# Kernel optimization log

Hardware: AMD Instinct MI355X
Metric: run time of the kernel (lower is better)

Reference implementation:

```python
import jax, jax.numpy as jnp
import numpy as np

# Hardware-emulation constants (from init_kwargs, NeuroSim-style QLinear)
WL_IN = 8        # input activation bit width (bit-serial)
WL_W = 8         # weight bit width
CELL_BIT = 2     # bits per memory cell -> 4 weight slices
SUB = 128        # crossbar sub-array size (rows summed in analog)
ADC_BITS = 5     # ADC precision per partial sum
ONOFF = 10.0     # cell on/off conductance ratio
VARI = 0.05      # multiplicative device variation sigma


def _adc_quant(x, bits, axes):
    # LinearQuantizeOut: uniform quantization between tensor min/max
    mn = jnp.min(x, axis=axes, keepdims=True)
    mx = jnp.max(x, axis=axes, keepdims=True)
    step = (mx - mn) * (2.0 ** (-bits))
    step = jnp.where(step <= 0, 1.0, step)
    idx = jnp.clip(jnp.floor((x - mn) / step), 0.0, 2.0 ** bits - 1.0)
    return idx * step + mn


def _qlinear_hw(x, w, noise):
    """Analog PIM crossbar emulation of y = x @ w.T with bit-serial inputs,
    bit-sliced cells, on/off-ratio offset + dummy column, device variation,
    per-subarray ADC quantization."""
    B, N = x.shape
    F = w.shape[0]
    I, W, K = WL_IN, WL_W, WL_W // CELL_BIT
    cr = 2.0 ** CELL_BIT
    lower, upper = 1.0 / ONOFF, 1.0
    S = (N + SUB - 1) // SUB
    Np = S * SUB
    # quantize input to I bits in [0,1]; weight to W-bit integer in [0, 2^W-1]
    xq = jnp.round(jnp.clip(x, 0.0, 1.0) * (2.0 ** I - 1.0))            # [B, N]
    Xi = jnp.clip(jnp.round((w + 1.0) * 0.5 * (2.0 ** W - 1.0)), 0.0, 2.0 ** W - 1.0)  # [F, N]
    xq = jnp.pad(xq, ((0, 0), (0, Np - N)))
    Xi = jnp.pad(Xi, ((0, 0), (0, Np - N)))
    zpow = 2.0 ** jnp.arange(I, dtype=x.dtype)
    kpow = cr ** jnp.arange(K, dtype=x.dtype)
    bits = jnp.mod(jnp.floor(xq[..., None] / zpow), 2.0)                # [B, Np, I]
    slc = jnp.mod(jnp.floor(Xi[..., None] / kpow), cr)                  # [F, Np, K]
    g = slc * (upper - lower) + (cr - 1.0) * lower                      # cell conductances
    g = g * (1.0 + VARI * noise)                                        # device variation
    bits = bits.reshape(B, S, SUB, I)
    g = g.reshape(F, S, SUB, K)
    # analog partial sums per (input bit i, subarray s, weight slice k)
    P = jnp.einsum('bsai,fsak->iskbf', bits, g)                         # [I,S,K,B,F]
    # dummy column (all cells at lowest conductance), identical across F
    D = jnp.transpose(bits.sum(axis=2), (2, 1, 0)) * ((cr - 1.0) * lower)  # [I,S,B]
    Pq = _adc_quant(P, ADC_BITS, axes=(3, 4))
    Dq = _adc_quant(D, ADC_BITS, axes=(2,))
    scal = (2.0 ** jnp.arange(I, dtype=x.dtype))[:, None] * (cr ** jnp.arange(K, dtype=x.dtype))[None, :]
    acc = jnp.einsum('iskbf,ik->bf', Pq - Dq[:, :, None, :, None], scal) / (upper - lower)
    # undo integer mappings: w = 2*Xi/(2^W-1) - 1, x = xq/(2^I-1)
    out = 2.0 * acc / ((2.0 ** I - 1.0) * (2.0 ** W - 1.0)) \
          - xq.sum(axis=1, keepdims=True) / (2.0 ** I - 1.0)
    return out


def _qlinear(x, w, noise):
    # straight-through quantized weight (WAGE-style STE) + hardware forward
    Xi = jnp.clip(jnp.round((w + 1.0) * 0.5 * (2.0 ** WL_W - 1.0)), 0.0, 2.0 ** WL_W - 1.0)
    wq = 2.0 * Xi / (2.0 ** WL_W - 1.0) - 1.0
    wq_ste = w + jax.lax.stop_gradient(wq - w)
    out_ideal = x @ wq_ste.T
    out_hw = _qlinear_hw(x, w, noise)
    return out_ideal + jax.lax.stop_gradient(out_hw - out_ideal)


def setup_inputs() -> dict:
    key = jax.random.key(0)
    k1, k2, k3, k4, k5 = jax.random.split(key, 5)
    x = jax.random.uniform(k1, (1024, 784), dtype=jnp.float32)
    w1 = jax.random.normal(k2, (512, 784), dtype=jnp.float32) * 0.05
    w3 = jax.random.normal(k3, (10, 512), dtype=jnp.float32) * 0.08
    noise1 = jax.random.normal(k4, (512, 896, 4), dtype=jnp.float32)  # 784 padded to 7*128
    noise3 = jax.random.normal(k5, (10, 512, 4), dtype=jnp.float32)   # 512 = 4*128 exact
    return {"x": x, "w1": w1, "w3": w3, "noise1": noise1, "noise3": noise3}


def reference(x, w1, w3, noise1, noise3):
    h = jnp.tanh(_qlinear(x, w1, noise1))   # QLinear(784,512) + Tanh
    return _qlinear(h, w3, noise3)          # QLinear(512,10)
```

## Files before the change

kernel.cpp:

```cpp
#include <hip/hip_runtime.h>

#define FLTMAX 3.402823466e+38f


__global__ void prep1_kernel(const float* __restrict__ x, float* __restrict__ sx1,
                             unsigned* __restrict__ xqbT, unsigned* __restrict__ stats1)
{
    __shared__ float xr[896];
    __shared__ float red[128];
    int b = blockIdx.x;
    if (b == 0) {
        for (int t = threadIdx.x; t < 224; t += 128) {
            stats1[t * 2] = 0x7F7FFFFFu; stats1[t * 2 + 1] = 0u;
        }
    }
    float psum = 0.f;
    for (int n = threadIdx.x; n < 896; n += 128) {
        float v = 0.f;
        if (n < 784) {
            float xv = x[b * 784 + n];
            xv = fminf(fmaxf(xv, 0.f), 1.f);
            v = rintf(__fmul_rn(xv, 255.f));
        }
        xr[n] = v;
        psum += v;
    }
    red[threadIdx.x] = psum;
    __syncthreads();
    for (int w = 64; w >= 1; w >>= 1) {
        if (threadIdx.x < w) red[threadIdx.x] += red[threadIdx.x + w];
        __syncthreads();
    }
    if (threadIdx.x == 0) sx1[b] = red[0];
    if (threadIdx.x < 28) {
        int w = threadIdx.x;
        unsigned words[8] = {0, 0, 0, 0, 0, 0, 0, 0};
#pragma unroll 8
        for (int n = 0; n < 32; ++n) {
            int v = (int)xr[w * 32 + n];
#pragma unroll
            for (int i = 0; i < 8; ++i) words[i] |= ((unsigned)((v >> i) & 1)) << n;
        }
#pragma unroll
        for (int i = 0; i < 8; ++i) xqbT[(i * 28 + w) * 1024 + b] = words[i];
    }
}

__global__ void prepg1t_kernel(const float* __restrict__ w1, const float* __restrict__ noise1,
                               float* __restrict__ g1t)
{
    __shared__ float t[4][32][33];
    const int n0 = blockIdx.x * 32, f0 = blockIdx.y * 32;
    const int tid = threadIdx.x;
    {
        int n = tid & 31, fi = tid >> 5;
#pragma unroll
        for (int p = 0; p < 4; ++p) {
            int f = p * 8 + fi;
            int gn = n0 + n, gf = f0 + f;
            float gv[4] = {0.f, 0.f, 0.f, 0.f};
            if (gn < 784) {
                float w = w1[gf * 784 + gn];
                float Xi = fminf(fmaxf(rintf(__fmul_rn(__fmul_rn(__fadd_rn(w, 1.f), 0.5f), 255.f)),
                                       0.f), 255.f);
                int xi = (int)Xi;
                float4 nz = *(const float4*)&noise1[(gf * 896 + gn) * 4];
                float nzv[4] = {nz.x, nz.y, nz.z, nz.w};
#pragma unroll
                for (int k = 0; k < 4; ++k) {
                    int slc = (xi >> (2 * k)) & 3;
                    float base = __fadd_rn(__fmul_rn((float)slc, 0.9f), 0.3f);
                    float nf = __fadd_rn(1.f, __fmul_rn(0.05f, nzv[k]));
                    gv[k] = __fmul_rn(base, nf);
                }
            }
#pragma unroll
            for (int k = 0; k < 4; ++k) t[k][n][f] = gv[k];
        }
    }
    __syncthreads();
    {
        int f = tid & 31, nn = tid >> 5;
#pragma unroll
        for (int p = 0; p < 4; ++p) {
            int n = p * 8 + nn;
#pragma unroll
            for (int k = 0; k < 4; ++k)
                g1t[(n0 + n) * 2048 + k * 512 + f0 + f] = t[k][n][f];
        }
    }
}

__global__ void prepg2_kernel(const float* __restrict__ w3, const float* __restrict__ noise3,
                              float* __restrict__ g2t)
{
    int gid = blockIdx.x * 256 + threadIdx.x;
    if (gid >= 10 * 512) return;
    int f = gid / 512, n = gid % 512;
    float w = w3[f * 512 + n];
    float Xi = fminf(fmaxf(rintf(__fmul_rn(__fmul_rn(__fadd_rn(w, 1.f), 0.5f), 255.f)),
                           0.f), 255.f);
    int xi = (int)Xi;
#pragma unroll
    for (int k = 0; k < 4; ++k) {
        int slc = (xi >> (2 * k)) & 3;
        float base = __fadd_rn(__fmul_rn((float)slc, 0.9f), 0.3f);
        float nf = __fadd_rn(1.f, __fmul_rn(0.05f, noise3[(f * 512 + n) * 4 + k]));
        g2t[n * 40 + k * 10 + f] = __fmul_rn(base, nf);
    }
}

__global__ void dqpopT_kernel(const unsigned* __restrict__ xqbT, float* __restrict__ Dq)
{
    __shared__ float red[512];
    const int i = blockIdx.x / 7, s = blockIdx.x % 7;
    const int tid = threadIdx.x;
    float D[4];
    float mn = FLTMAX, mx = -FLTMAX;
#pragma unroll
    for (int u = 0; u < 4; ++u) {
        int b = tid + u * 256;
        int c = 0;
#pragma unroll
        for (int w = 0; w < 4; ++w)
            c += __popc(xqbT[(i * 28 + s * 4 + w) * 1024 + b]);
        D[u] = __fmul_rn((float)c, 0.3f);
        mn = fminf(mn, D[u]);
        mx = fmaxf(mx, D[u]);
    }
    red[tid] = mn; red[256 + tid] = mx;
    __syncthreads();
    for (int w = 128; w >= 1; w >>= 1) {
        if (tid < w) {
            red[tid] = fminf(red[tid], red[tid + w]);
            red[256 + tid] = fmaxf(red[256 + tid], red[256 + tid + w]);
        }
        __syncthreads();
    }
    mn = red[0]; mx = red[256];
    float step = __fmul_rn(__fsub_rn(mx, mn), 0.03125f);
    if (step <= 0.f) step = 1.f;
#pragma unroll
    for (int u = 0; u < 4; ++u) {
        int b = tid + u * 256;
        float idx = fminf(fmaxf(floorf(__fdiv_rn(__fsub_rn(D[u], mn), step)), 0.f), 31.f);
        Dq[(i * 7 + s) * 1024 + b] = __fadd_rn(__fmul_rn(idx, step), mn);
    }
}

__global__ void dqpop_kernel(const unsigned* __restrict__ xqb, float* __restrict__ Dq,
                             int S, int wpr)
{
    __shared__ float red[512];
    const int i = blockIdx.x / S, s = blockIdx.x % S;
    const int tid = threadIdx.x;
    float D[4];
    float mn = FLTMAX, mx = -FLTMAX;
#pragma unroll
    for (int u = 0; u < 4; ++u) {
        int b = tid + u * 256;
        uint4 w = *(const uint4*)&xqb[(i * 1024 + b) * wpr + s * 4];
        int c = __popc(w.x) + __popc(w.y) + __popc(w.z) + __popc(w.w);
        D[u] = __fmul_rn((float)c, 0.3f);
        mn = fminf(mn, D[u]);
        mx = fmaxf(mx, D[u]);
    }
    red[tid] = mn; red[256 + tid] = mx;
    __syncthreads();
    for (int w = 128; w >= 1; w >>= 1) {
        if (tid < w) {
            red[tid] = fminf(red[tid], red[tid + w]);
            red[256 + tid] = fmaxf(red[256 + tid], red[256 + tid + w]);
        }
        __syncthreads();
    }
    mn = red[0]; mx = red[256];
    float step = __fmul_rn(__fsub_rn(mx, mn), 0.03125f);
    if (step <= 0.f) step = 1.f;
#pragma unroll
    for (int u = 0; u < 4; ++u) {
        int b = tid + u * 256;
        float idx = fminf(fmaxf(floorf(__fdiv_rn(__fsub_rn(D[u], mn), step)), 0.f), 31.f);
        Dq[(i * S + s) * 1024 + b] = __fadd_rn(__fmul_rn(idx, step), mn);
    }
}

__global__ void dterm_kernel(const float* __restrict__ Dq, float* __restrict__ dterm, int S)
{
    int b = blockIdx.x * 256 + threadIdx.x;
    if (b >= 1024) return;
    float sum = 0.f;
    for (int i = 0; i < 8; ++i) {
        float sc = (float)(85 << i);
        for (int s = 0; s < S; ++s) sum = fmaf(Dq[(i * S + s) * 1024 + b], sc, sum);
    }
    dterm[b] = sum;
}

#define BK 32
__global__ __launch_bounds__(256, 4) void mm1_kernel(
    const unsigned* __restrict__ xqbT, const float* __restrict__ g1t,
    float* __restrict__ P, unsigned* __restrict__ stats, int s0)
{
    __shared__ __align__(16) float Bs[BK][132];
    __shared__ unsigned Abits[128];
    __shared__ float red[512];
    const int tid = threadIdx.x;
    const int sl = blockIdx.x >> 6;
    const int r = blockIdx.x & 63;
    const int i = r >> 3;
    const int b0 = (r & 7) * 128;
    const int s = s0 + sl;
    const int colBase = blockIdx.y * 128;
    const int tx = tid & 15, ty = tid >> 4;

    const int aB = tid >> 5;
    const int eB = (tid & 31) << 2;

    float4 pB[4];
    unsigned pAw = 0;
#pragma unroll
    for (int u = 0; u < 4; ++u)
        pB[u] = *(const float4*)&g1t[(s * 128 + u * 8 + aB) * 2048 + colBase + eB];
    if (tid < 128) pAw = xqbT[(i * 28 + s * 4) * 1024 + b0 + tid];

    float acc[8][8] = {};

    for (int ac = 0; ac < 4; ++ac) {
        __syncthreads();
#pragma unroll
        for (int u = 0; u < 4; ++u)
            *(float4*)&Bs[u * 8 + aB][eB] = pB[u];
        if (tid < 128) Abits[tid] = pAw;
        __syncthreads();

        if (ac < 3) {
            const int n0 = s * 128 + (ac + 1) * BK;
#pragma unroll
            for (int u = 0; u < 4; ++u)
                pB[u] = *(const float4*)&g1t[(n0 + u * 8 + aB) * 2048 + colBase + eB];
            if (tid < 128) pAw = xqbT[(i * 28 + s * 4 + ac + 1) * 1024 + b0 + tid];
        }

        unsigned wrd[8];
#pragma unroll
        for (int u = 0; u < 4; ++u) {
            wrd[u]     = Abits[(ty << 2) + u];
            wrd[4 + u] = Abits[64 + (ty << 2) + u];
        }

#pragma unroll 4
        for (int a = 0; a < BK; ++a) {
            float br[8];
            *(float4*)&br[0] = *(const float4*)&Bs[a][(tx << 2)];
            *(float4*)&br[4] = *(const float4*)&Bs[a][64 + (tx << 2)];
#pragma unroll
            for (int u = 0; u < 8; ++u) {
                float ab = (float)((wrd[u] >> a) & 1u);
#pragma unroll
                for (int v = 0; v < 8; ++v)
                    acc[u][v] = fmaf(ab, br[v], acc[u][v]);
            }
        }
    }

#pragma unroll
    for (int uh = 0; uh < 2; ++uh)
#pragma unroll
        for (int u = 0; u < 4; ++u) {
            int row = (sl * 8 + i) * 1024 + b0 + uh * 64 + (ty << 2) + u;
#pragma unroll
            for (int vh = 0; vh < 2; ++vh) {
                float4 v = make_float4(acc[uh * 4 + u][vh * 4 + 0], acc[uh * 4 + u][vh * 4 + 1],
                                       acc[uh * 4 + u][vh * 4 + 2], acc[uh * 4 + u][vh * 4 + 3]);
                *(float4*)&P[(size_t)row * 2048 + colBase + vh * 64 + (tx << 2)] = v;
            }
        }

    float mn = acc[0][0], mx = acc[0][0];
#pragma unroll
    for (int u = 0; u < 8; ++u)
#pragma unroll
        for (int v = 0; v < 8; ++v) { mn = fminf(mn, acc[u][v]); mx = fmaxf(mx, acc[u][v]); }
    red[tid] = mn; red[256 + tid] = mx;
    __syncthreads();
    for (int w = 128; w >= 1; w >>= 1) {
        if (tid < w) {
            red[tid] = fminf(red[tid], red[tid + w]);
            red[256 + tid] = fmaxf(red[256 + tid], red[256 + tid + w]);
        }
        __syncthreads();
    }
    if (tid == 0) {
        int k = colBase >> 9;
        int slot = ((s * 8 + i) * 4 + k) * 2;
        atomicMin(&stats[slot], __float_as_uint(red[0]));
        atomicMax(&stats[slot + 1], __float_as_uint(red[256]));
    }
}

__global__ void quant1_kernel(const float* __restrict__ P, const unsigned* __restrict__ stats,
                              float* __restrict__ acc1, int s0, int G, int first)
{
    int gid = blockIdx.x * 256 + threadIdx.x;
    int b = gid >> 7, f4 = gid & 127;
    float4 accR;
    if (first) accR = make_float4(0.f, 0.f, 0.f, 0.f);
    else       accR = *(const float4*)&acc1[(b << 9) + (f4 << 2)];
    for (int sl = 0; sl < G; ++sl) {
        int s = s0 + sl;
        float4 sum = make_float4(0.f, 0.f, 0.f, 0.f);
        for (int i = 0; i < 8; ++i) {
#pragma unroll
            for (int k = 0; k < 4; ++k) {
                int slot = ((s * 8 + i) * 4 + k) * 2;
                float mn = __uint_as_float(stats[slot]);
                float mx = __uint_as_float(stats[slot + 1]);
                float step = __fmul_rn(__fsub_rn(mx, mn), 0.03125f);
                if (step <= 0.f) step = 1.f;
                float4 val = *(const float4*)&P[(size_t)((sl * 8 + i) * 1024 + b) * 2048
                                                + (k << 9) + (f4 << 2)];
                float sc = (float)(1 << (i + 2 * k));
                float ix, pq;
                ix = fminf(fmaxf(floorf(__fdiv_rn(__fsub_rn(val.x, mn), step)), 0.f), 31.f);
                pq = __fadd_rn(__fmul_rn(ix, step), mn); sum.x = fmaf(pq, sc, sum.x);
                ix = fminf(fmaxf(floorf(__fdiv_rn(__fsub_rn(val.y, mn), step)), 0.f), 31.f);
                pq = __fadd_rn(__fmul_rn(ix, step), mn); sum.y = fmaf(pq, sc, sum.y);
                ix = fminf(fmaxf(floorf(__fdiv_rn(__fsub_rn(val.z, mn), step)), 0.f), 31.f);
                pq = __fadd_rn(__fmul_rn(ix, step), mn); sum.z = fmaf(pq, sc, sum.z);
                ix = fminf(fmaxf(floorf(__fdiv_rn(__fsub_rn(val.w, mn), step)), 0.f), 31.f);
                pq = __fadd_rn(__fmul_rn(ix, step), mn); sum.w = fmaf(pq, sc, sum.w);
            }
        }
        accR.x = __fadd_rn(accR.x, sum.x);
        accR.y = __fadd_rn(accR.y, sum.y);
        accR.z = __fadd_rn(accR.z, sum.z);
        accR.w = __fadd_rn(accR.w, sum.w);
    }
    *(float4*)&acc1[(b << 9) + (f4 << 2)] = accR;
}

__global__ void finish1_kernel(const float* __restrict__ acc1, const float* __restrict__ dterm1,
                               const float* __restrict__ sx1, float* __restrict__ xq2,
                               unsigned* __restrict__ xqb2, float* __restrict__ sx2)
{
    __shared__ float red[512];
    int b = blockIdx.x;
    int f = threadIdx.x;
    int gid = b * 512 + f;
    float total = __fsub_rn(acc1[gid], dterm1[b]);
    float acc = __fdiv_rn(total, 0.9f);
    float o = __fsub_rn(__fdiv_rn(__fmul_rn(2.f, acc), 65025.f), __fdiv_rn(sx1[b], 255.f));
    float h = tanhf(o);
    h = fminf(fmaxf(h, 0.f), 1.f);
    float code = rintf(__fmul_rn(h, 255.f));
    xq2[gid] = code;
    int ci = (int)code;
    int lane = f & 63;
#pragma unroll
    for (int i = 0; i < 8; ++i) {
        unsigned long long m = __ballot((ci >> i) & 1);
        if ((lane & 31) == 0) {
            unsigned wv = (lane & 32) ? (unsigned)(m >> 32) : (unsigned)m;
            xqb2[(i * 1024 + b) * 16 + (f >> 5)] = wv;
        }
    }
    red[f] = code;
    __syncthreads();
    for (int w = 256; w >= 1; w >>= 1) {
        if (f < w) red[f] += red[f + w];
        __syncthreads();
    }
    if (f == 0) sx2[b] = red[0];
}

__global__ void mm2_kernel(const float* __restrict__ xq2, const float* __restrict__ g2t,
                           float* __restrict__ P2)
{
    int gid = blockIdx.x * 256 + threadIdx.x;
    if (gid >= 40960) return;
    int f = gid % 10;
    int b = (gid / 10) & 1023;
    int s = gid / 10240;
    float acc[8][4] = {};
    for (int a = 0; a < 128; ++a) {
        int n = s * 128 + a;
        int xi = (int)xq2[b * 512 + n];
        float g0 = g2t[n * 40 + f];
        float gA = g2t[n * 40 + 10 + f];
        float gB = g2t[n * 40 + 20 + f];
        float gC = g2t[n * 40 + 30 + f];
#pragma unroll
        for (int i = 0; i < 8; ++i) {
            float bi = (float)((xi >> i) & 1);
            acc[i][0] = fmaf(bi, g0, acc[i][0]);
            acc[i][1] = fmaf(bi, gA, acc[i][1]);
            acc[i][2] = fmaf(bi, gB, acc[i][2]);
            acc[i][3] = fmaf(bi, gC, acc[i][3]);
        }
    }
#pragma unroll
    for (int i = 0; i < 8; ++i)
#pragma unroll
        for (int k = 0; k < 4; ++k)
            P2[(size_t)((s * 8 + i) * 4 + k) * 10240 + b * 10 + f] = acc[i][k];
}

__global__ void stat2_kernel(const float* __restrict__ P2, float2* __restrict__ stats2)
{
    __shared__ float red[512];
    int p = blockIdx.x;
    int tid = threadIdx.x;
    float mn = FLTMAX, mx = -FLTMAX;
    for (int t = tid; t < 10240; t += 256) {
        float v = P2[(size_t)p * 10240 + t];
        mn = fminf(mn, v); mx = fmaxf(mx, v);
    }
    red[tid] = mn; red[256 + tid] = mx;
    __syncthreads();
    for (int w = 128; w >= 1; w >>= 1) {
        if (tid < w) {
            red[tid] = fminf(red[tid], red[tid + w]);
            red[256 + tid] = fmaxf(red[256 + tid], red[256 + tid + w]);
        }
        __syncthreads();
    }
    if (tid == 0) {
        float step = __fmul_rn(__fsub_rn(red[256], red[0]), 0.03125f);
        if (step <= 0.f) step = 1.f;
        stats2[p] = make_float2(red[0], step);
    }
}

__global__ void out2_kernel(const float* __restrict__ P2, const float2* __restrict__ stats2,
                            const float* __restrict__ dterm2, const float* __restrict__ sx2,
                            float* __restrict__ out)
{
    int gid = blockIdx.x * 256 + threadIdx.x;
    if (gid >= 10240) return;
    int b = gid / 10;
    float sum = 0.f;
    for (int s = 0; s < 4; ++s)
        for (int i = 0; i < 8; ++i)
#pragma unroll
            for (int k = 0; k < 4; ++k) {
                int p = (s * 8 + i) * 4 + k;
                float2 st = stats2[p];
                float val = P2[(size_t)p * 10240 + gid];
                float idx = fminf(fmaxf(floorf(__fdiv_rn(__fsub_rn(val, st.x), st.y)), 0.f), 31.f);
                float pq = __fadd_rn(__fmul_rn(idx, st.y), st.x);
                sum = fmaf(pq, (float)(1 << (i + 2 * k)), sum);
            }
    float total = __fsub_rn(sum, dterm2[b]);
    float acc = __fdiv_rn(total, 0.9f);
    out[gid] = __fsub_rn(__fdiv_rn(__fmul_rn(2.f, acc), 65025.f), __fdiv_rn(sx2[b], 255.f));
}

extern "C" void kernel_launch(void* const* d_in, const int* in_sizes, int n_in,
                              void* d_out, int out_size, void* d_ws, size_t ws_size,
                              hipStream_t stream)
{
    const float* x      = (const float*)d_in[0];
    const float* w1     = (const float*)d_in[1];
    const float* w3     = (const float*)d_in[2];
    const float* noise1 = (const float*)d_in[3];
    const float* noise3 = (const float*)d_in[4];
    float* out = (float*)d_out;
    float* ws  = (float*)d_ws;

    float*    g1t    = ws + 0;
    float*    acc1   = ws + 1835008;
    float*    xq2    = ws + 2359296;
    float*    P2     = ws + 2883584;
    float*    g2t    = ws + 4194304;
    float*    Dq1    = ws + 4214784;
    float*    Dq2    = ws + 4272128;
    float*    sx1    = ws + 4304896;
    float*    sx2    = ws + 4305920;
    float*    dterm1 = ws + 4306944;
    float*    dterm2 = ws + 4307968;
    float2*   stats2 = (float2*)(ws + 4308992);
    unsigned* stats1 = (unsigned*)(ws + 4309248);
    unsigned* xqbT   = (unsigned*)(ws + 4309760);
    unsigned* xqb2   = (unsigned*)(ws + 4539136);
    float*    Ps     = ws + 4670208;

    const size_t fixedf = 4670208;
    const size_t planef = 16777216;
    int G = ((fixedf + 2 * planef) * sizeof(float) <= ws_size) ? 2 : 1;

    prep1_kernel<<<1024, 128, 0, stream>>>(x, sx1, xqbT, stats1);
    prepg1t_kernel<<<dim3(28, 16), 256, 0, stream>>>(w1, noise1, g1t);
    dqpopT_kernel<<<56, 256, 0, stream>>>(xqbT, Dq1);
    dterm_kernel<<<4, 256, 0, stream>>>(Dq1, dterm1, 7);

    for (int s0 = 0; s0 < 7; s0 += G) {
        int Gc = (7 - s0 < G) ? (7 - s0) : G;
        mm1_kernel<<<dim3(Gc * 64, 16), 256, 0, stream>>>(xqbT, g1t, Ps, stats1, s0);
        quant1_kernel<<<512, 256, 0, stream>>>(Ps, stats1, acc1, s0, Gc, s0 == 0);
    }

    finish1_kernel<<<1024, 512, 0, stream>>>(acc1, dterm1, sx1, xq2, xqb2, sx2);
    prepg2_kernel<<<20, 256, 0, stream>>>(w3, noise3, g2t);
    dqpop_kernel<<<32, 256, 0, stream>>>(xqb2, Dq2, 4, 16);
    dterm_kernel<<<4, 256, 0, stream>>>(Dq2, dterm2, 4);
    mm2_kernel<<<160, 256, 0, stream>>>(xq2, g2t, P2);
    stat2_kernel<<<128, 256, 0, stream>>>(P2, stats2);
    out2_kernel<<<40, 256, 0, stream>>>(P2, stats2, dterm2, sx2, out);
}
```

Measured before the change: 670.4 us.

## Fuse dterm and last quant pass into finish kernels, grow subarray group size

Removes the two dterm kernels by computing the dummy-column term inside finish1 (one thread per row) and out2 (per thread). The last quant1 pass is folded into finish1, which now dequantizes the final group of partial-sum planes directly. The group count G can now grow up to 7 when workspace allows, so fewer mm1/quant1 launch pairs run. The cost is a serial 56-load loop on one thread per block in finish1, redundant dterm loads per thread in out2, and finish1 reading a large P plane strided by 2048.

```diff
diff --git a/kernel.cpp b/kernel.cpp
--- a/kernel.cpp
+++ b/kernel.cpp
@@ -183,18 +183,6 @@
         float idx = fminf(fmaxf(floorf(__fdiv_rn(__fsub_rn(D[u], mn), step)), 0.f), 31.f);
         Dq[(i * S + s) * 1024 + b] = __fadd_rn(__fmul_rn(idx, step), mn);
     }
-}
-
-__global__ void dterm_kernel(const float* __restrict__ Dq, float* __restrict__ dterm, int S)
-{
-    int b = blockIdx.x * 256 + threadIdx.x;
-    if (b >= 1024) return;
-    float sum = 0.f;
-    for (int i = 0; i < 8; ++i) {
-        float sc = (float)(85 << i);
-        for (int s = 0; s < S; ++s) sum = fmaf(Dq[(i * S + s) * 1024 + b], sc, sum);
-    }
-    dterm[b] = sum;
 }
 
 #define BK 32
@@ -340,15 +328,47 @@
     *(float4*)&acc1[(b << 9) + (f4 << 2)] = accR;
 }
 
-__global__ void finish1_kernel(const float* __restrict__ acc1, const float* __restrict__ dterm1,
-                               const float* __restrict__ sx1, float* __restrict__ xq2,
-                               unsigned* __restrict__ xqb2, float* __restrict__ sx2)
+__global__ void finish1_kernel(const float* __restrict__ acc1, const float* __restrict__ P,
+                               const unsigned* __restrict__ stats, int s0, int G, int first,
+                               const float* __restrict__ Dq1, const float* __restrict__ sx1,
+                               float* __restrict__ xq2, unsigned* __restrict__ xqb2,
+                               float* __restrict__ sx2)
 {
     __shared__ float red[512];
+    __shared__ float dt;
     int b = blockIdx.x;
     int f = threadIdx.x;
+    if (f == 0) {
+        float s = 0.f;
+        for (int i = 0; i < 8; ++i) {
+            float sc = (float)(85 << i);
+            for (int ss = 0; ss < 7; ++ss) s = fmaf(Dq1[(i * 7 + ss) * 1024 + b], sc, s);
+        }
+        dt = s;
+    }
+    __syncthreads();
     int gid = b * 512 + f;
-    float total = __fsub_rn(acc1[gid], dterm1[b]);
+    float accR = first ? 0.f : acc1[gid];
+    for (int sl = 0; sl < G; ++sl) {
+        int s = s0 + sl;
+        float sum = 0.f;
+        for (int i = 0; i < 8; ++i) {
+#pragma unroll
+            for (int k = 0; k < 4; ++k) {
+                int slot = ((s * 8 + i) * 4 + k) * 2;
+                float mn = __uint_as_float(stats[slot]);
+                float mx = __uint_as_float(stats[slot + 1]);
+                float step = __fmul_rn(__fsub_rn(mx, mn), 0.03125f);
+                if (step <= 0.f) step = 1.f;
+                float val = P[(size_t)((sl * 8 + i) * 1024 + b) * 2048 + (k << 9) + f];
+                float ix = fminf(fmaxf(floorf(__fdiv_rn(__fsub_rn(val, mn), step)), 0.f), 31.f);
+                float pq = __fadd_rn(__fmul_rn(ix, step), mn);
+                sum = fmaf(pq, (float)(1 << (i + 2 * k)), sum);
+            }
+        }
+        accR = __fadd_rn(accR, sum);
+    }
+    float total = __fsub_rn(accR, dt);
     float acc = __fdiv_rn(total, 0.9f);
     float o = __fsub_rn(__fdiv_rn(__fmul_rn(2.f, acc), 65025.f), __fdiv_rn(sx1[b], 255.f));
     float h = tanhf(o);
@@ -433,12 +453,17 @@
 }
 
 __global__ void out2_kernel(const float* __restrict__ P2, const float2* __restrict__ stats2,
-                            const float* __restrict__ dterm2, const float* __restrict__ sx2,
+                            const float* __restrict__ Dq2, const float* __restrict__ sx2,
                             float* __restrict__ out)
 {
     int gid = blockIdx.x * 256 + threadIdx.x;
     if (gid >= 10240) return;
     int b = gid / 10;
+    float dt = 0.f;
+    for (int i = 0; i < 8; ++i) {
+        float sc = (float)(85 << i);
+        for (int s = 0; s < 4; ++s) dt = fmaf(Dq2[(i * 4 + s) * 1024 + b], sc, dt);
+    }
     float sum = 0.f;
     for (int s = 0; s < 4; ++s)
         for (int i = 0; i < 8; ++i)
@@ -451,7 +476,7 @@
                 float pq = __fadd_rn(__fmul_rn(idx, st.y), st.x);
                 sum = fmaf(pq, (float)(1 << (i + 2 * k)), sum);
             }
-    float total = __fsub_rn(sum, dterm2[b]);
+    float total = __fsub_rn(sum, dt);
     float acc = __fdiv_rn(total, 0.9f);
     out[gid] = __fsub_rn(__fdiv_rn(__fmul_rn(2.f, acc), 65025.f), __fdiv_rn(sx2[b], 255.f));
 }
@@ -477,34 +502,39 @@
     float*    Dq2    = ws + 4272128;
     float*    sx1    = ws + 4304896;
     float*    sx2    = ws + 4305920;
-    float*    dterm1 = ws + 4306944;
-    float*    dterm2 = ws + 4307968;
-    float2*   stats2 = (float2*)(ws + 4308992);
-    unsigned* stats1 = (unsigned*)(ws + 4309248);
-    unsigned* xqbT   = (unsigned*)(ws + 4309760);
-    unsigned* xqb2   = (unsigned*)(ws + 4539136);
-    float*    Ps     = ws + 4670208;
-
-    const size_t fixedf = 4670208;
+    float2*   stats2 = (float2*)(ws + 4306944);
+    unsigned* stats1 = (unsigned*)(ws + 4307200);
+    unsigned* xqbT   = (unsigned*)(ws + 4307712);
+    unsigned* xqb2   = (unsigned*)(ws + 4537088);
+    float*    Ps     = ws + 4668160;
+
+    const size_t fixedf = 4668160;
     const size_t planef = 16777216;
-    int G = ((fixedf + 2 * planef) * sizeof(float) <= ws_size) ? 2 : 1;
+    int G = 1;
+    while (G < 7 && (fixedf + (size_t)(G + 1) * planef) * sizeof(float) <= ws_size) ++G;
 
     prep1_kernel<<<1024, 128, 0, stream>>>(x, sx1, xqbT, stats1);
     prepg1t_kernel<<<dim3(28, 16), 256, 0, stream>>>(w1, noise1, g1t);
     dqpopT_kernel<<<56, 256, 0, stream>>>(xqbT, Dq1);
-    dterm_kernel<<<4, 256, 0, stream>>>(Dq1, dterm1, 7);
-
-    for (int s0 = 0; s0 < 7; s0 += G) {
+
+    int lastS0 = 0, lastG = 7, anyQuant = 0;
+    for (int s0 = 0; s0 < 7;) {
         int Gc = (7 - s0 < G) ? (7 - s0) : G;
         mm1_kernel<<<dim3(Gc * 64, 16), 256, 0, stream>>>(xqbT, g1t, Ps, stats1, s0);
-        quant1_kernel<<<512, 256, 0, stream>>>(Ps, stats1, acc1, s0, Gc, s0 == 0);
-    }
-
-    finish1_kernel<<<1024, 512, 0, stream>>>(acc1, dterm1, sx1, xq2, xqb2, sx2);
+        if (s0 + Gc < 7) {
+            quant1_kernel<<<512, 256, 0, stream>>>(Ps, stats1, acc1, s0, Gc, s0 == 0);
+            anyQuant = 1;
+        } else {
+            lastS0 = s0; lastG = Gc;
+        }
+        s0 += Gc;
+    }
+
+    finish1_kernel<<<1024, 512, 0, stream>>>(acc1, Ps, stats1, lastS0, lastG,
+                                             anyQuant ? 0 : 1, Dq1, sx1, xq2, xqb2, sx2);
     prepg2_kernel<<<20, 256, 0, stream>>>(w3, noise3, g2t);
     dqpop_kernel<<<32, 256, 0, stream>>>(xqb2, Dq2, 4, 16);
-    dterm_kernel<<<4, 256, 0, stream>>>(Dq2, dterm2, 4);
     mm2_kernel<<<160, 256, 0, stream>>>(xq2, g2t, P2);
     stat2_kernel<<<128, 256, 0, stream>>>(P2, stats2);
-    out2_kernel<<<40, 256, 0, stream>>>(P2, stats2, dterm2, sx2, out);
-}
+    out2_kernel<<<40, 256, 0, stream>>>(P2, stats2, Dq2, sx2, out);
+}
```

New measurement: 632.0 us. -5.7%, faster.
